# Performance work log

Hardware: AMD Instinct MI355X
Metric: run time of the kernel (lower is better)

Reference implementation:

```python
import jax, jax.numpy as jnp
import numpy as np

N = 100000
E = 1600000
IN_DIM = 128
H = 64
OUT_DIM = 64
EPS = 1e-5


def batch_norm(x, gamma, beta):
    # BatchNorm1d with batch statistics (training-mode normalization, biased var)
    mu = jnp.mean(x, axis=0)
    var = jnp.var(x, axis=0)
    return (x - mu) * jax.lax.rsqrt(var + EPS) * gamma + beta


def gcn_conv(x, src, dst, W, b, n_nodes):
    # PyG GCNConv: add self-loops, symmetric deg^-1/2 normalization, X W, scatter-add, bias
    loop = jnp.arange(n_nodes, dtype=src.dtype)
    s = jnp.concatenate([src, loop])
    d = jnp.concatenate([dst, loop])
    w = jnp.ones(s.shape[0], dtype=x.dtype)
    deg = jax.ops.segment_sum(w, d, num_segments=n_nodes)
    dinv = jnp.where(deg > 0, jax.lax.rsqrt(deg), 0.0)
    norm = dinv[s] * w * dinv[d]                      # [E+N]
    h = x @ W                                         # [N, out]
    msg = h[s] * norm[:, None]                        # [E+N, out]
    out = jax.ops.segment_sum(msg, d, num_segments=n_nodes)
    return out + b


def setup_inputs() -> dict:
    key = jax.random.key(0)
    ks = jax.random.split(key, 12)
    x = jax.random.normal(ks[0], (N, IN_DIM), dtype=jnp.float32)
    edge_index = jax.random.randint(ks[1], (2, E), 0, N, dtype=jnp.int64)
    s = 0.05
    return {
        "x": x,
        "edge_index": edge_index,
        "bn_in_g": jnp.ones((IN_DIM,), jnp.float32),
        "bn_in_b": jnp.zeros((IN_DIM,), jnp.float32),
        "Wp": jax.random.normal(ks[2], (IN_DIM, H), jnp.float32) * s,
        "bp": jnp.zeros((H,), jnp.float32),
        "W1": jax.random.normal(ks[3], (H, H), jnp.float32) * s,
        "b1": jnp.zeros((H,), jnp.float32),
        "bn1_g": jnp.ones((H,), jnp.float32),
        "bn1_b": jnp.zeros((H,), jnp.float32),
        "W2": jax.random.normal(ks[4], (H, OUT_DIM), jnp.float32) * s,
        "b2": jnp.zeros((OUT_DIM,), jnp.float32),
        "bn2_g": jnp.ones((OUT_DIM,), jnp.float32),
        "bn2_b": jnp.zeros((OUT_DIM,), jnp.float32),
    }


def reference(x, edge_index, bn_in_g, bn_in_b, Wp, bp, W1, b1, bn1_g, bn1_b, W2, b2, bn2_g, bn2_b):
    src, dst = edge_index[0], edge_index[1]
    n = x.shape[0]
    h0 = batch_norm(x, bn_in_g, bn_in_b)
    h0 = jax.nn.relu(h0 @ Wp + bp)
    h1 = gcn_conv(h0, src, dst, W1, b1, n)
    h1 = jax.nn.relu(batch_norm(h1, bn1_g, bn1_b))
    # dropout in eval mode: identity
    h2 = gcn_conv(h1, src, dst, W2, b2, n)
    return batch_norm(h2, bn2_g, bn2_b)
```

## Files before the change

kernel.cpp:

```cpp
#include <hip/hip_runtime.h>
#include <hip/hip_bf16.h>

#define EPS 1e-5f

__device__ __forceinline__ void acc_q(float* acc, uint2 v, float s) {
    acc[0] += s * (float)((int)(v.x << 24) >> 24);
    acc[1] += s * (float)((int)(v.x << 16) >> 24);
    acc[2] += s * (float)((int)(v.x << 8) >> 24);
    acc[3] += s * (float)((int)v.x >> 24);
    acc[4] += s * (float)((int)(v.y << 24) >> 24);
    acc[5] += s * (float)((int)(v.y << 16) >> 24);
    acc[6] += s * (float)((int)(v.y << 8) >> 24);
    acc[7] += s * (float)((int)v.y >> 24);
}

__global__ __launch_bounds__(256) void k_pre(const int* __restrict__ dst,
                                             int* __restrict__ cc,
                                             const float* __restrict__ x,
                                             float* __restrict__ xsum,
                                             float* __restrict__ xsq,
                                             int E, int N, int NB) {
    __shared__ float lsf[512];
    int tx = threadIdx.x;
    if (blockIdx.x < 512) {
        int* h = (int*)lsf;
        for (int i = tx; i < NB; i += 256) h[i] = 0;
        __syncthreads();
        int stride = 512 * 256;
        for (int e = blockIdx.x * 256 + tx; e < E; e += stride)
            atomicAdd(&h[dst[e] >> 8], 1);
        __syncthreads();
        for (int i = tx; i < NB; i += 256)
            if (h[i]) atomicAdd(&cc[i], h[i]);
    } else {
        float* ls = lsf;
        float* lq = lsf + 256;
        int b2 = blockIdx.x - 512;
        int col = tx & 127, half = tx >> 7;
        float s = 0.f, q = 0.f;
        for (int r = b2 * 2 + half; r < N; r += 1024) {
            float v = x[(long long)r * 128 + col];
            s += v; q += v * v;
        }
        ls[tx] = s; lq[tx] = q;
        __syncthreads();
        if (half == 0) {
            s = ls[tx] + ls[tx + 128];
            q = lq[tx] + lq[tx + 128];
            atomicAdd(&xsum[col], s);
            atomicAdd(&xsq[col], q);
        }
    }
}

__global__ void k_cscan(const int* __restrict__ cc, int* __restrict__ coff,
                        int* __restrict__ cur, int NB, int E) {
    __shared__ int ls[512];
    int tx = threadIdx.x;
    int v = (tx < NB) ? cc[tx] : 0;
    ls[tx] = v;
    __syncthreads();
    for (int off = 1; off < 512; off <<= 1) {
        int u = (tx >= off) ? ls[tx - off] : 0;
        __syncthreads();
        ls[tx] += u;
        __syncthreads();
    }
    int excl = ls[tx] - v;
    if (tx < NB) { coff[tx] = excl; cur[tx] = excl; }
    if (tx == NB - 1) coff[NB] = excl + v;
}

#define PCHUNK 2048
__global__ __launch_bounds__(256) void k_mid(
    const int* __restrict__ src, const int* __restrict__ dst,
    int* __restrict__ cursor, unsigned* __restrict__ packbuf, int E, int NB, int PB,
    const float* __restrict__ x, const float* __restrict__ stats,
    const float* __restrict__ g, const float* __restrict__ bbn,
    const float* __restrict__ Wp, const float* __restrict__ bp,
    float* __restrict__ H, float invN, int N) {
    __shared__ int h[512], base[512];
    int tx = threadIdx.x;
    if (blockIdx.x < PB) {
        int e0 = blockIdx.x * PCHUNK;
        int e1 = min(e0 + PCHUNK, E);
        for (int i = tx; i < NB; i += 256) h[i] = 0;
        __syncthreads();
        for (int e = e0 + tx; e < e1; e += 256)
            atomicAdd(&h[dst[e] >> 8], 1);
        __syncthreads();
        for (int i = tx; i < NB; i += 256) {
            int c = h[i];
            base[i] = c ? atomicAdd(&cursor[i], c) : 0;
            h[i] = 0;
        }
        __syncthreads();
        for (int e = e0 + tx; e < e1; e += 256) {
            int d = dst[e];
            int b = d >> 8;
            int p = base[b] + atomicAdd(&h[b], 1);
            packbuf[p] = ((unsigned)src[e] << 8) | (unsigned)(d & 255);
        }
    } else {
        float* sc = (float*)h;
        float* sh = (float*)base;
        if (tx < 128) {
            float mu = stats[tx] * invN;
            float var = stats[128 + tx] * invN - mu * mu;
            float s = g[tx] * rsqrtf(var + EPS);
            sc[tx] = s;
            sh[tx] = bbn[tx] - mu * s;
        }
        __syncthreads();
        int r = (blockIdx.x - PB) * 256 + tx;
        if (r >= N) return;
        float acc[64];
#pragma unroll
        for (int j = 0; j < 64; j++) acc[j] = 0.f;
        const float4* x4 = (const float4*)(x + (long long)r * 128);
        for (int c4 = 0; c4 < 32; c4++) {
            float4 xv = x4[c4];
            int cb = c4 * 4;
            xv.x = xv.x * sc[cb + 0] + sh[cb + 0];
            xv.y = xv.y * sc[cb + 1] + sh[cb + 1];
            xv.z = xv.z * sc[cb + 2] + sh[cb + 2];
            xv.w = xv.w * sc[cb + 3] + sh[cb + 3];
#pragma unroll
            for (int q = 0; q < 4; q++) {
                float xs = (q == 0) ? xv.x : (q == 1) ? xv.y : (q == 2) ? xv.z : xv.w;
                const float* wrow = Wp + (c4 * 4 + q) * 64;
#pragma unroll
                for (int j = 0; j < 64; j++) acc[j] += xs * wrow[j];
            }
        }
        float4* out4 = (float4*)(H + (long long)r * 64);
#pragma unroll
        for (int i = 0; i < 16; i++) {
            float4 v;
            v.x = fmaxf(acc[4 * i + 0] + bp[4 * i + 0], 0.f);
            v.y = fmaxf(acc[4 * i + 1] + bp[4 * i + 1], 0.f);
            v.z = fmaxf(acc[4 * i + 2] + bp[4 * i + 2], 0.f);
            v.w = fmaxf(acc[4 * i + 3] + bp[4 * i + 3], 0.f);
            out4[i] = v;
        }
    }
}

__global__ __launch_bounds__(512) void k_build(const unsigned* __restrict__ packbuf,
                                               const int* __restrict__ coff,
                                               int* __restrict__ rowptr,
                                               float* __restrict__ dinv,
                                               int* __restrict__ eidx, int N, int E) {
    __shared__ int cnt[256], loff[256], wsum[4];
    int b = blockIdx.x;
    int tx = threadIdx.x;
    int beg = coff[b], end = coff[b + 1];
    if (tx < 256) cnt[tx] = 0;
    __syncthreads();
    for (int e = beg + tx; e < end; e += 512)
        atomicAdd(&cnt[packbuf[e] & 255u], 1);
    __syncthreads();
    if (tx < 256) {
        int c = cnt[tx];
        int lane = tx & 63, wid = tx >> 6;
        int v = c;
#pragma unroll
        for (int off = 1; off < 64; off <<= 1) {
            int u = __shfl_up(v, off);
            if (lane >= off) v += u;
        }
        if (lane == 63) wsum[wid] = v;
        __syncthreads();
        int wbase = 0;
        for (int w = 0; w < wid; w++) wbase += wsum[w];
        int excl = wbase + v - c;
        loff[tx] = excl;
        int node = b * 256 + tx;
        if (node < N) {
            rowptr[node] = beg + excl;
            dinv[node] = rsqrtf(1.0f + (float)c);
        }
    } else {
        __syncthreads();
    }
    if (b == 0 && tx == 0) rowptr[N] = E;
    __syncthreads();
    for (int e = beg + tx; e < end; e += 512) {
        unsigned pk = packbuf[e];
        int pos = atomicAdd(&loff[pk & 255u], 1);
        eidx[beg + pos] = (int)(pk >> 8);
    }
}

template <bool BNRELU>
__global__ __launch_bounds__(256) void k_gemm_scale(
    const float* __restrict__ In, const float* __restrict__ W,
    const float* __restrict__ dinv, const float* __restrict__ ssum,
    const float* __restrict__ ssq, const float* __restrict__ g,
    const float* __restrict__ bb, float invN, unsigned* __restrict__ Bq,
    float* __restrict__ S, int N) {
    __shared__ float scs[64], shs[64];
    int tx = threadIdx.x;
    if (BNRELU) {
        if (tx < 64) {
            float mu = ssum[tx] * invN;
            float var = ssq[tx] * invN - mu * mu;
            float s = g[tx] * rsqrtf(var + EPS);
            scs[tx] = s;
            shs[tx] = bb[tx] - mu * s;
        }
        __syncthreads();
    }
    int r = blockIdx.x * blockDim.x + tx;
    if (r >= N) return;
    float acc[64];
#pragma unroll
    for (int j = 0; j < 64; j++) acc[j] = 0.f;
    const float4* in4 = (const float4*)(In + (long long)r * 64);
    for (int c4 = 0; c4 < 16; c4++) {
        float4 xv = in4[c4];
        if (BNRELU) {
            int cb = c4 * 4;
            xv.x = fmaxf(xv.x * scs[cb + 0] + shs[cb + 0], 0.f);
            xv.y = fmaxf(xv.y * scs[cb + 1] + shs[cb + 1], 0.f);
            xv.z = fmaxf(xv.z * scs[cb + 2] + shs[cb + 2], 0.f);
            xv.w = fmaxf(xv.w * scs[cb + 3] + shs[cb + 3], 0.f);
        }
#pragma unroll
        for (int q = 0; q < 4; q++) {
            float xs = (q == 0) ? xv.x : (q == 1) ? xv.y : (q == 2) ? xv.z : xv.w;
            const float* wrow = W + (c4 * 4 + q) * 64;
#pragma unroll
            for (int j = 0; j < 64; j++) acc[j] += xs * wrow[j];
        }
    }
    float dv = dinv[r];
    float vmax = 0.f;
#pragma unroll
    for (int j = 0; j < 64; j++) {
        acc[j] *= dv;
        vmax = fmaxf(vmax, fabsf(acc[j]));
    }
    S[r] = vmax * (1.0f / 127.0f);
    float inv = (vmax > 0.f) ? (127.0f / vmax) : 0.f;
    uint4* b4 = (uint4*)(Bq + (long long)r * 16);
#pragma unroll
    for (int i = 0; i < 4; i++) {
        unsigned w[4];
#pragma unroll
        for (int k2 = 0; k2 < 4; k2++) {
            int bsx = i * 16 + k2 * 4;
            unsigned q0 = (unsigned)((int)rintf(acc[bsx + 0] * inv)) & 255u;
            unsigned q1 = (unsigned)((int)rintf(acc[bsx + 1] * inv)) & 255u;
            unsigned q2 = (unsigned)((int)rintf(acc[bsx + 2] * inv)) & 255u;
            unsigned q3 = (unsigned)((int)rintf(acc[bsx + 3] * inv)) & 255u;
            w[k2] = q0 | (q1 << 8) | (q2 << 16) | (q3 << 24);
        }
        b4[i] = make_uint4(w[0], w[1], w[2], w[3]);
    }
}

__global__ __launch_bounds__(256) void k_gather_finish(
    const uint2* __restrict__ B, const float* __restrict__ S,
    const int* __restrict__ rowptr, const int* __restrict__ eidx,
    const float* __restrict__ dinv, const float* __restrict__ bias,
    float* __restrict__ Out, float* __restrict__ ssum, float* __restrict__ ssq, int N) {
    int tx = threadIdx.x;
    int g = tx >> 3;
    int l = tx & 7;
    int d = blockIdx.x * 32 + g;

    float s[8], q[8];
#pragma unroll
    for (int j = 0; j < 8; j++) { s[j] = 0.f; q[j] = 0.f; }

    if (d < N) {
        int beg = rowptr[d], end = rowptr[d + 1];
        float acc[8];
#pragma unroll
        for (int j = 0; j < 8; j++) acc[j] = 0.f;
        {
            uint2 v0 = B[(long long)d * 8 + l];
            float s0 = S[d];
            acc_q(acc, v0, s0);
        }
        int k = beg;
        for (; k + 3 < end; k += 4) {
            int i0 = eidx[k + 0], i1 = eidx[k + 1], i2 = eidx[k + 2], i3 = eidx[k + 3];
            uint2 a0 = B[(long long)i0 * 8 + l];
            uint2 a1 = B[(long long)i1 * 8 + l];
            uint2 a2 = B[(long long)i2 * 8 + l];
            uint2 a3 = B[(long long)i3 * 8 + l];
            float s0 = S[i0], s1 = S[i1], s2 = S[i2], s3 = S[i3];
            acc_q(acc, a0, s0); acc_q(acc, a1, s1);
            acc_q(acc, a2, s2); acc_q(acc, a3, s3);
        }
        for (; k + 1 < end; k += 2) {
            int i0 = eidx[k + 0], i1 = eidx[k + 1];
            uint2 a0 = B[(long long)i0 * 8 + l];
            uint2 a1 = B[(long long)i1 * 8 + l];
            float s0 = S[i0], s1 = S[i1];
            acc_q(acc, a0, s0); acc_q(acc, a1, s1);
        }
        if (k < end) {
            int i0 = eidx[k];
            uint2 a0 = B[(long long)i0 * 8 + l];
            acc_q(acc, a0, S[i0]);
        }
        float dv = dinv[d];
        float4 o0, o1;
#pragma unroll
        for (int j = 0; j < 8; j++) {
            float v = acc[j] * dv + bias[8 * l + j];
            ((j < 4) ? (&o0.x)[j] : (&o1.x)[j - 4]) = v;
            s[j] += v; q[j] += v * v;
        }
        float4* outp = (float4*)(Out + (long long)d * 64 + 8 * l);
        outp[0] = o0;
        outp[1] = o1;
    }

#pragma unroll
    for (int m = 8; m <= 32; m <<= 1) {
#pragma unroll
        for (int j = 0; j < 8; j++) {
            s[j] += __shfl_xor(s[j], m, 64);
            q[j] += __shfl_xor(q[j], m, 64);
        }
    }
    __shared__ float ws_s[4][64], ws_q[4][64];
    int wv = tx >> 6, ln = tx & 63;
    if (ln < 8) {
#pragma unroll
        for (int j = 0; j < 8; j++) {
            ws_s[wv][ln * 8 + j] = s[j];
            ws_q[wv][ln * 8 + j] = q[j];
        }
    }
    __syncthreads();
    if (tx < 64) {
        float S2 = ws_s[0][tx] + ws_s[1][tx] + ws_s[2][tx] + ws_s[3][tx];
        float Q2 = ws_q[0][tx] + ws_q[1][tx] + ws_q[2][tx] + ws_q[3][tx];
        atomicAdd(&ssum[tx], S2);
        atomicAdd(&ssq[tx], Q2);
    }
}

__global__ __launch_bounds__(256) void k_final(const float* __restrict__ In,
                                               const float* __restrict__ ssum,
                                               const float* __restrict__ ssq,
                                               const float* __restrict__ g,
                                               const float* __restrict__ bb, float invN,
                                               float* __restrict__ out, int total4) {
    __shared__ float scs[64], shs[64];
    int tx = threadIdx.x;
    if (tx < 64) {
        float mu = ssum[tx] * invN;
        float var = ssq[tx] * invN - mu * mu;
        float s = g[tx] * rsqrtf(var + EPS);
        scs[tx] = s;
        shs[tx] = bb[tx] - mu * s;
    }
    __syncthreads();
    int t = blockIdx.x * blockDim.x + tx;
    if (t < total4) {
        float4 v = ((const float4*)In)[t];
        int j = (t * 4) & 63;
        v.x = v.x * scs[j + 0] + shs[j + 0];
        v.y = v.y * scs[j + 1] + shs[j + 1];
        v.z = v.z * scs[j + 2] + shs[j + 2];
        v.w = v.w * scs[j + 3] + shs[j + 3];
        ((float4*)out)[t] = v;
    }
}

extern "C" void kernel_launch(void* const* d_in, const int* in_sizes, int n_in,
                              void* d_out, int out_size, void* d_ws, size_t ws_size,
                              hipStream_t stream) {
    const float* x       = (const float*)d_in[0];
    const int*   ei      = (const int*)d_in[1];
    const float* bn_in_g = (const float*)d_in[2];
    const float* bn_in_b = (const float*)d_in[3];
    const float* Wp      = (const float*)d_in[4];
    const float* bp      = (const float*)d_in[5];
    const float* W1      = (const float*)d_in[6];
    const float* b1      = (const float*)d_in[7];
    const float* bn1_g   = (const float*)d_in[8];
    const float* bn1_b   = (const float*)d_in[9];
    const float* W2      = (const float*)d_in[10];
    const float* b2      = (const float*)d_in[11];
    const float* bn2_g   = (const float*)d_in[12];
    const float* bn2_b   = (const float*)d_in[13];

    int N = in_sizes[0] / 128;
    int E = in_sizes[1] / 2;
    const int* src = ei;
    const int* dst = ei + E;
    int NB = (N + 255) >> 8;

    long long Npad = ((long long)N + 128) & ~127LL;
    int*   cc     = (int*)d_ws;
    float* stats  = (float*)(cc + 512);
    int*   coff   = (int*)(stats + 512);
    int*   cur    = coff + 640;
    int*   rowptr = cur + 512;
    float* dinv   = (float*)(rowptr + Npad);
    float* S      = dinv + Npad;
    unsigned* packbuf = (unsigned*)(S + Npad);
    int*   eidx   = (int*)(packbuf + ((E + 127) & ~127));
    unsigned* Bq  = (unsigned*)(eidx + ((E + 127) & ~127));
    float* H      = (float*)d_out;

    int nb = (N + 255) / 256;
    int gb = (N + 31) / 32;
    int PB = (E + PCHUNK - 1) / PCHUNK;
    float invN = 1.0f / (float)N;

    hipMemsetAsync(d_ws, 0, (512 + 512) * 4, stream);

    k_pre<<<1024, 256, 0, stream>>>(dst, cc, x, stats, stats + 128, E, N, NB);
    k_cscan<<<1, 512, 0, stream>>>(cc, coff, cur, NB, E);
    k_mid<<<PB + nb, 256, 0, stream>>>(src, dst, cur, packbuf, E, NB, PB,
                                       x, stats, bn_in_g, bn_in_b, Wp, bp, H, invN, N);
    k_build<<<NB, 512, 0, stream>>>(packbuf, coff, rowptr, dinv, eidx, N, E);

    k_gemm_scale<false><<<nb, 256, 0, stream>>>(H, W1, dinv, nullptr, nullptr, nullptr,
                                                nullptr, invN, Bq, S, N);
    k_gather_finish<<<gb, 256, 0, stream>>>((const uint2*)Bq, S, rowptr, eidx, dinv,
                                            b1, H, stats + 256, stats + 320, N);

    k_gemm_scale<true><<<nb, 256, 0, stream>>>(H, W2, dinv, stats + 256, stats + 320,
                                               bn1_g, bn1_b, invN, Bq, S, N);
    k_gather_finish<<<gb, 256, 0, stream>>>((const uint2*)Bq, S, rowptr, eidx, dinv,
                                            b2, H, stats + 384, stats + 448, N);

    k_final<<<(N * 16 + 255) / 256, 256, 0, stream>>>(H, stats + 384, stats + 448,
                                                      bn2_g, bn2_b, invN, H, N * 16);
}
```

Measured before the change: 495.0 us.

## Stage bucketed edge packing in shared memory for coalesced global writes

The edge-bucketing part of k_mid now scatters packed edges into a shared-memory buffer in bucket order, using a block-local prefix scan over bucket counts. It then writes them out contiguously, using a binary search to map each position to its global bucket offset. The aim is to turn random scattered global stores into mostly sequential runs. The chunk size doubles to 4096 edges per block, which raises shared memory use and lowers the number of blocks. It also adds scan and binary-search work and lowers occupancy for the non-packing blocks.

```diff
diff --git a/kernel.cpp b/kernel.cpp
--- a/kernel.cpp
+++ b/kernel.cpp
@@ -71,7 +71,7 @@
     if (tx == NB - 1) coff[NB] = excl + v;
 }
 
-#define PCHUNK 2048
+#define PCHUNK 4096
 __global__ __launch_bounds__(256) void k_mid(
     const int* __restrict__ src, const int* __restrict__ dst,
     int* __restrict__ cursor, unsigned* __restrict__ packbuf, int E, int NB, int PB,
@@ -79,31 +79,62 @@
     const float* __restrict__ g, const float* __restrict__ bbn,
     const float* __restrict__ Wp, const float* __restrict__ bp,
     float* __restrict__ H, float invN, int N) {
-    __shared__ int h[512], base[512];
+    __shared__ int h[512], start[520], delta[512];
+    __shared__ unsigned buf[PCHUNK];
     int tx = threadIdx.x;
     if (blockIdx.x < PB) {
         int e0 = blockIdx.x * PCHUNK;
         int e1 = min(e0 + PCHUNK, E);
-        for (int i = tx; i < NB; i += 256) h[i] = 0;
+        int csize = e1 - e0;
+        h[tx] = 0; h[tx + 256] = 0;
         __syncthreads();
         for (int e = e0 + tx; e < e1; e += 256)
             atomicAdd(&h[dst[e] >> 8], 1);
         __syncthreads();
-        for (int i = tx; i < NB; i += 256) {
-            int c = h[i];
-            base[i] = c ? atomicAdd(&cursor[i], c) : 0;
-            h[i] = 0;
-        }
+        start[tx] = h[tx]; start[tx + 256] = h[tx + 256];
+        __syncthreads();
+        for (int off = 1; off < 512; off <<= 1) {
+            int i0 = tx, i1 = tx + 256;
+            int v0 = (i0 >= off) ? start[i0 - off] : 0;
+            int v1 = (i1 >= off) ? start[i1 - off] : 0;
+            __syncthreads();
+            start[i0] += v0; start[i1] += v1;
+            __syncthreads();
+        }
+#pragma unroll
+        for (int t = 0; t < 2; t++) {
+            int b = tx + t * 256;
+            int c = h[b];
+            int excl = start[b] - c;
+            if (b < NB) {
+                int gbase = c ? atomicAdd(&cursor[b], c) : 0;
+                delta[b] = gbase - excl;
+            }
+            start[b] = excl;
+        }
+        __syncthreads();
+        h[tx] = start[tx]; h[tx + 256] = start[tx + 256];
+        if (tx == 0) start[NB] = csize;
         __syncthreads();
         for (int e = e0 + tx; e < e1; e += 256) {
             int d = dst[e];
             int b = d >> 8;
-            int p = base[b] + atomicAdd(&h[b], 1);
-            packbuf[p] = ((unsigned)src[e] << 8) | (unsigned)(d & 255);
+            int rank = atomicAdd(&h[b], 1);
+            buf[rank] = ((unsigned)src[e] << 8) | (unsigned)(d & 255);
+        }
+        __syncthreads();
+        for (int i = tx; i < csize; i += 256) {
+            unsigned pk = buf[i];
+            int lo = 0, hi = NB;
+            while (hi - lo > 1) {
+                int mid = (lo + hi) >> 1;
+                if (start[mid] <= i) lo = mid; else hi = mid;
+            }
+            packbuf[delta[lo] + i] = pk;
         }
     } else {
         float* sc = (float*)h;
-        float* sh = (float*)base;
+        float* sh = (float*)delta;
         if (tx < 128) {
             float mu = stats[tx] * invN;
             float var = stats[128 + tx] * invN - mu * mu;
@@ -281,8 +312,7 @@
         for (int j = 0; j < 8; j++) acc[j] = 0.f;
         {
             uint2 v0 = B[(long long)d * 8 + l];
-            float s0 = S[d];
-            acc_q(acc, v0, s0);
+            acc_q(acc, v0, S[d]);
         }
         int k = beg;
         for (; k + 3 < end; k += 4) {
```

New measurement: 483.2 us. 2.4% less time.

## Stage edge bucketing in shared memory for coalesced packbuf writes

Applied to the files above, without the earlier changes.

The edge-partition phase of k_mid now does a block-local exclusive scan of the bucket counts. It places each packed edge into a shared-memory buffer in bucket order, then writes the buffer to global memory contiguously per bucket. This replaces scattered per-edge global writes with runs of consecutive addresses. The chunk size doubles to 4096 edges per block, so there are fewer cursor atomics but also fewer partition blocks. The extra ~16KB+ of shared memory per block may reduce occupancy for the fused BN+matmul blocks that share this kernel.

```diff
diff --git a/kernel.cpp b/kernel.cpp
--- a/kernel.cpp
+++ b/kernel.cpp
@@ -71,7 +71,7 @@
     if (tx == NB - 1) coff[NB] = excl + v;
 }
 
-#define PCHUNK 2048
+#define PCHUNK 4096
 __global__ __launch_bounds__(256) void k_mid(
     const int* __restrict__ src, const int* __restrict__ dst,
     int* __restrict__ cursor, unsigned* __restrict__ packbuf, int E, int NB, int PB,
@@ -79,31 +79,53 @@
     const float* __restrict__ g, const float* __restrict__ bbn,
     const float* __restrict__ Wp, const float* __restrict__ bp,
     float* __restrict__ H, float invN, int N) {
-    __shared__ int h[512], base[512];
+    __shared__ int h[512], delta[512], wsc[4];
+    __shared__ unsigned buf[PCHUNK];
+    __shared__ int addr[PCHUNK];
     int tx = threadIdx.x;
     if (blockIdx.x < PB) {
         int e0 = blockIdx.x * PCHUNK;
         int e1 = min(e0 + PCHUNK, E);
-        for (int i = tx; i < NB; i += 256) h[i] = 0;
+        int csize = e1 - e0;
+        h[tx] = 0; h[tx + 256] = 0;
         __syncthreads();
         for (int e = e0 + tx; e < e1; e += 256)
             atomicAdd(&h[dst[e] >> 8], 1);
         __syncthreads();
-        for (int i = tx; i < NB; i += 256) {
-            int c = h[i];
-            base[i] = c ? atomicAdd(&cursor[i], c) : 0;
-            h[i] = 0;
-        }
+        int b0 = tx * 2;
+        int c0 = h[b0], c1 = h[b0 + 1];
+        int tsum = c0 + c1;
+        int lane = tx & 63, wid = tx >> 6;
+        int v = tsum;
+#pragma unroll
+        for (int off = 1; off < 64; off <<= 1) {
+            int u = __shfl_up(v, off);
+            if (lane >= off) v += u;
+        }
+        if (lane == 63) wsc[wid] = v;
+        __syncthreads();
+        int wbase = 0;
+        for (int w = 0; w < wid; w++) wbase += wsc[w];
+        int excl0 = wbase + v - tsum;
+        int excl1 = excl0 + c0;
+        if (b0 < NB && c0 > 0) delta[b0] = atomicAdd(&cursor[b0], c0) - excl0;
+        if (b0 + 1 < NB && c1 > 0) delta[b0 + 1] = atomicAdd(&cursor[b0 + 1], c1) - excl1;
+        __syncthreads();
+        h[b0] = excl0; h[b0 + 1] = excl1;
         __syncthreads();
         for (int e = e0 + tx; e < e1; e += 256) {
             int d = dst[e];
             int b = d >> 8;
-            int p = base[b] + atomicAdd(&h[b], 1);
-            packbuf[p] = ((unsigned)src[e] << 8) | (unsigned)(d & 255);
-        }
+            int rank = atomicAdd(&h[b], 1);
+            buf[rank] = ((unsigned)src[e] << 8) | (unsigned)(d & 255);
+            addr[rank] = delta[b];
+        }
+        __syncthreads();
+        for (int i = tx; i < csize; i += 256)
+            packbuf[addr[i] + i] = buf[i];
     } else {
         float* sc = (float*)h;
-        float* sh = (float*)base;
+        float* sh = (float*)delta;
         if (tx < 128) {
             float mu = stats[tx] * invN;
             float var = stats[128 + tx] * invN - mu * mu;
@@ -136,12 +158,12 @@
         float4* out4 = (float4*)(H + (long long)r * 64);
 #pragma unroll
         for (int i = 0; i < 16; i++) {
-            float4 v;
-            v.x = fmaxf(acc[4 * i + 0] + bp[4 * i + 0], 0.f);
-            v.y = fmaxf(acc[4 * i + 1] + bp[4 * i + 1], 0.f);
-            v.z = fmaxf(acc[4 * i + 2] + bp[4 * i + 2], 0.f);
-            v.w = fmaxf(acc[4 * i + 3] + bp[4 * i + 3], 0.f);
-            out4[i] = v;
+            float4 vv;
+            vv.x = fmaxf(acc[4 * i + 0] + bp[4 * i + 0], 0.f);
+            vv.y = fmaxf(acc[4 * i + 1] + bp[4 * i + 1], 0.f);
+            vv.z = fmaxf(acc[4 * i + 2] + bp[4 * i + 2], 0.f);
+            vv.w = fmaxf(acc[4 * i + 3] + bp[4 * i + 3], 0.f);
+            out4[i] = vv;
         }
     }
 }
@@ -281,8 +303,7 @@
         for (int j = 0; j < 8; j++) acc[j] = 0.f;
         {
             uint2 v0 = B[(long long)d * 8 + l];
-            float s0 = S[d];
-            acc_q(acc, v0, s0);
+            acc_q(acc, v0, S[d]);
         }
         int k = beg;
         for (; k + 3 < end; k += 4) {
```

After: 482.7 us. 2.5% less time.
